# Optimization experiments

Hardware: AMD Instinct MI355X
Metric: run time of the kernel (lower is better)

## Reference

```python
import jax, jax.numpy as jnp
import numpy as np

TOP_K = 16
TAU = 1.0
LN_EPS = 1e-5
NORM_EPS = 1e-12


def setup_inputs() -> dict:
    key = jax.random.key(0)
    ks = jax.random.split(key, 8)
    B, T, V, H = 2, 1024, 32000, 1024
    inner = 2 * H
    logits = jax.random.normal(ks[0], (B, T, V), jnp.float32)
    hidden_states = jax.random.normal(ks[1], (B, T, H), jnp.float32)
    labels = jax.random.randint(ks[2], (B, T), 0, V, jnp.int32)
    future_summaries = jax.random.normal(ks[3], (B, T, H), jnp.float32)
    future_valid = jnp.ones((B, T), jnp.bool_)
    embed_weight = jax.random.normal(ks[4], (V, H), jnp.float32) * 0.02
    W1 = jax.random.normal(ks[5], (2 * H, inner), jnp.float32) * 0.02
    b1 = jnp.zeros((inner,), jnp.float32)
    W2 = jax.random.normal(ks[6], (inner, H), jnp.float32) * 0.02
    b2 = jnp.zeros((H,), jnp.float32)
    ln_g = jnp.ones((H,), jnp.float32)
    ln_b = jnp.zeros((H,), jnp.float32)
    return dict(logits=logits, hidden_states=hidden_states, labels=labels,
                future_summaries=future_summaries, future_valid=future_valid,
                embed_weight=embed_weight, W1=W1, b1=b1, W2=W2, b2=b2,
                ln_g=ln_g, ln_b=ln_b)


def _build_action_set(logits_flat, labels_flat):
    # top-k candidate ids + ground-truth id, deduped, left-packed.
    BT = logits_flat.shape[0]
    _, topk_idx = jax.lax.top_k(logits_flat, TOP_K)          # (BT, K)
    combined = jnp.concatenate([topk_idx, labels_flat[:, None]], axis=1)  # (BT, A)
    A = combined.shape[1]
    sort_order = jnp.argsort(combined, axis=1)               # stable
    sorted_idx = jnp.take_along_axis(combined, sort_order, axis=1)
    uniq_sorted = jnp.concatenate(
        [jnp.ones((BT, 1), jnp.bool_), sorted_idx[:, 1:] != sorted_idx[:, :-1]], axis=1)
    unsort = jnp.argsort(sort_order, axis=1)
    unique_mask = jnp.take_along_axis(uniq_sorted, unsort, axis=1)
    pos = jnp.cumsum(unique_mask, axis=1) - 1
    # route duplicates to a trash column A, then slice it off
    safe_pos = jnp.where(unique_mask, pos, A)
    rows = jnp.arange(BT)[:, None]
    action_indices = jnp.zeros((BT, A + 1), combined.dtype).at[rows, safe_pos].set(combined)[:, :A]
    action_mask = jnp.zeros((BT, A + 1), jnp.bool_).at[rows, safe_pos].set(True)[:, :A]
    return action_indices, action_mask


def _layernorm(x, g, b):
    mu = jnp.mean(x, axis=-1, keepdims=True)
    var = jnp.var(x, axis=-1, keepdims=True)
    return (x - mu) * jax.lax.rsqrt(var + LN_EPS) * g + b


def _normalize(x):
    n = jnp.linalg.norm(x, axis=-1, keepdims=True)
    return x / jnp.maximum(n, NORM_EPS)


def reference(logits, hidden_states, labels, future_summaries, future_valid,
              embed_weight, W1, b1, W2, b2, ln_g, ln_b):
    B, T, V = logits.shape
    H = hidden_states.shape[-1]
    logits_flat = logits.reshape(-1, V)
    hidden_flat = hidden_states.reshape(-1, H)
    labels_flat = labels.reshape(-1)
    future_flat = future_summaries.reshape(-1, H)
    valid_mask = (labels_flat != -100) & future_valid.reshape(-1)

    action_indices, action_mask = _build_action_set(
        jax.lax.stop_gradient(logits_flat), labels_flat)      # (BT, A)

    token_embeds = embed_weight[action_indices]               # (BT, A, H)
    A = token_embeds.shape[1]
    hidden_exp = jnp.broadcast_to(hidden_flat[:, None, :], token_embeds.shape)
    future_exp = jnp.broadcast_to(future_flat[:, None, :], token_embeds.shape)

    # cos_mlp head: Linear(2H, 2H) -> GELU -> Linear(2H, H) -> LayerNorm
    fused = jnp.concatenate([hidden_exp, token_embeds], axis=-1)  # (BT, A, 2H)
    h = jax.nn.gelu(jnp.einsum('baf,fi->bai', fused, W1) + b1, approximate=False)
    delta = jnp.einsum('bai,ih->bah', h, W2) + b2
    action_repr = _layernorm(delta, ln_g, ln_b)

    scores = jnp.sum(_normalize(action_repr) * _normalize(future_exp), axis=-1)  # (BT, A)
    scores = jnp.where(action_mask, scores, -1e9)
    rewards = jax.nn.softmax(scores / TAU, axis=-1) * action_mask

    act_mask_v = action_mask & valid_mask[:, None]
    log_probs = jax.nn.log_softmax(logits_flat, axis=-1)
    lp_actions = jnp.take_along_axis(log_probs, action_indices, axis=1) * act_mask_v
    loss_per_pos = -jnp.sum(jax.lax.stop_gradient(rewards) * lp_actions, axis=1)
    denom = jnp.maximum(jnp.sum(act_mask_v, axis=1), 1)
    loss_per_pos = loss_per_pos / denom * valid_mask.astype(jnp.float32)
    normalizer = jnp.maximum(jnp.sum(valid_mask.astype(jnp.float32)), 1.0)
    loss = jnp.sum(loss_per_pos) / normalizer
    return loss
```

## Files before the change

kernel.cpp:

```cpp
#include <hip/hip_runtime.h>
#include <hip/hip_bf16.h>
#include <math.h>

#define BTOT 2048
#define VV 32000
#define HH 1024
#define INNER 2048
#define NA 17
#define MTOT (BTOT * NA)
#define CAP 1088

typedef __bf16 bf16;
typedef __bf16 bf16x8 __attribute__((ext_vector_type(8)));
typedef float f32x4 __attribute__((ext_vector_type(4)));

__device__ __forceinline__ f32x4 mfma16(bf16x8 a, bf16x8 b, f32x4 c) {
    return __builtin_amdgcn_mfma_f32_16x16x32_bf16(a, b, c, 0, 0, 0);
}

__device__ __forceinline__ void gload16(const void* g, void* l) {
    __builtin_amdgcn_global_load_lds(
        (const __attribute__((address_space(1))) unsigned int*)g,
        (__attribute__((address_space(3))) unsigned int*)l, 16, 0, 0);
}

__device__ __forceinline__ bool vi_better(float va, int ia, float vb, int ib) {
    return (va > vb) || (va == vb && ia < ib);
}

__global__ __launch_bounds__(256)
void transpose_to_bf16(const float* __restrict__ src, bf16* __restrict__ dst,
                       int R, int C)
{
    __shared__ float tile[32][33];
    const int bx = blockIdx.x * 32;
    const int by = blockIdx.y * 32;
    const int tx = threadIdx.x;
    const int ty = threadIdx.y;
#pragma unroll
    for (int i = 0; i < 32; i += 8)
        tile[ty + i][tx] = src[(size_t)(by + ty + i) * C + bx + tx];
    __syncthreads();
#pragma unroll
    for (int i = 0; i < 32; i += 8)
        dst[(size_t)(bx + ty + i) * R + by + tx] = (bf16)tile[tx][ty + i];
}

__global__ __launch_bounds__(256)
void cast_hidden_kernel(const float* __restrict__ hidden, bf16* __restrict__ hb)
{
    const size_t i = ((size_t)blockIdx.x * 256 + threadIdx.x) * 8;
    float4 v0 = ((const float4*)(hidden + i))[0];
    float4 v1 = ((const float4*)(hidden + i))[1];
    bf16x8 o;
    o[0] = (bf16)v0.x; o[1] = (bf16)v0.y; o[2] = (bf16)v0.z; o[3] = (bf16)v0.w;
    o[4] = (bf16)v1.x; o[5] = (bf16)v1.y; o[6] = (bf16)v1.z; o[7] = (bf16)v1.w;
    *(bf16x8*)(hb + i) = o;
}

__global__ __launch_bounds__(256)
void topk_lse_kernel(const float* __restrict__ logits,
                     const int* __restrict__ labels,
                     const unsigned char* __restrict__ future_valid,
                     int* __restrict__ actions,
                     int* __restrict__ amask,
                     float* __restrict__ lp,
                     int* __restrict__ rvalid,
                     int* __restrict__ validcount)
{
    const int r = blockIdx.x;
    const int t = threadIdx.x;
    const float* __restrict__ lrow = logits + (size_t)r * VV;

    __shared__ float s_cv[CAP];
    __shared__ int   s_ci[CAP];
    __shared__ float candv[256];
    __shared__ int   candi[256];
    __shared__ float s_topv[16];
    __shared__ int   s_topi[16];
    __shared__ int   s_wtid;
    __shared__ int   s_cnt;
    __shared__ float s_redv[256];
    __shared__ int   s_redi[256];
    __shared__ int   s_redp[256];

    float m1 = -INFINITY, m2 = -INFINITY;
    int   i1 = 0x7fffffff, i2 = 0x7fffffff;
    const float4* __restrict__ lrow4 = (const float4*)lrow;
    for (int i = 0; i < 32; ++i) {
        int i4 = t + 256 * i;
        if (i4 < VV / 4) {
            float4 xv = lrow4[i4];
            float xs[4] = {xv.x, xv.y, xv.z, xv.w};
#pragma unroll
            for (int cc = 0; cc < 4; ++cc) {
                float x = xs[cc];
                int idx = i4 * 4 + cc;
                bool b1 = x > m1;
                bool b2 = x > m2;
                float nm2 = b1 ? m1 : (b2 ? x : m2);
                int   ni2 = b1 ? i1 : (b2 ? idx : i2);
                m1 = b1 ? x : m1;
                i1 = b1 ? idx : i1;
                m2 = nm2; i2 = ni2;
            }
        }
    }
    candv[t] = m1; candi[t] = i1;
    if (t == 0) s_cnt = 0;
    __syncthreads();

    int cur = 0;
    for (int round = 0; round < 16; ++round) {
        if (t < 64) {
            float bv = -INFINITY; int bi = 0x7fffffff; int btid = -1;
#pragma unroll
            for (int k2 = 0; k2 < 4; ++k2) {
                int tid = t + 64 * k2;
                float v = candv[tid]; int ii = candi[tid];
                if (vi_better(v, ii, bv, bi)) { bv = v; bi = ii; btid = tid; }
            }
#pragma unroll
            for (int ms = 1; ms < 64; ms <<= 1) {
                float ov = __shfl_xor(bv, ms, 64);
                int   oi = __shfl_xor(bi, ms, 64);
                int   ot = __shfl_xor(btid, ms, 64);
                if (vi_better(ov, oi, bv, bi)) { bv = ov; bi = oi; btid = ot; }
            }
            if (t == 0) { s_topv[round] = bv; s_topi[round] = bi; s_wtid = btid; }
        }
        __syncthreads();
        if (t == s_wtid) {
            ++cur;
            candv[t] = (cur < 2) ? m2 : -INFINITY;
            candi[t] = (cur < 2) ? i2 : 0x7fffffff;
        }
        __syncthreads();
    }

    const float M  = s_topv[0];
    const float Tv = s_topv[15];
    const int   Ti = s_topi[15];

    float lsum = 0.f;
    for (int i = 0; i < 32; ++i) {
        int i4 = t + 256 * i;
        if (i4 < VV / 4) {
            float4 xv = lrow4[i4];
            float xs[4] = {xv.x, xv.y, xv.z, xv.w};
#pragma unroll
            for (int cc = 0; cc < 4; ++cc) {
                float x = xs[cc];
                int idx = i4 * 4 + cc;
                lsum += __expf(x - M);
                if (!vi_better(Tv, Ti, x, idx)) {
                    int p = atomicAdd(&s_cnt, 1);
                    if (p < CAP) { s_cv[p] = x; s_ci[p] = idx; }
                }
            }
        }
    }
    s_redv[t] = lsum;
    __syncthreads();
    for (int s = 128; s > 0; s >>= 1) {
        if (t < s) s_redv[t] += s_redv[t + s];
        __syncthreads();
    }
    const float lse = M + logf(s_redv[0]);
    int C = s_cnt; if (C > CAP) C = CAP;
    __syncthreads();

    for (int round = 0; round < 16; ++round) {
        float bv = -INFINITY; int bi = 0x7fffffff; int bp = -1;
        for (int j = t; j < C; j += 256) {
            float v = s_cv[j]; int ii = s_ci[j];
            if (vi_better(v, ii, bv, bi)) { bv = v; bi = ii; bp = j; }
        }
        s_redv[t] = bv; s_redi[t] = bi; s_redp[t] = bp;
        __syncthreads();
        if (t < 64) {
#pragma unroll
            for (int k2 = 1; k2 < 4; ++k2) {
                float v = s_redv[t + 64*k2]; int ii = s_redi[t + 64*k2];
                int pp = s_redp[t + 64*k2];
                if (vi_better(v, ii, bv, bi)) { bv = v; bi = ii; bp = pp; }
            }
#pragma unroll
            for (int ms = 1; ms < 64; ms <<= 1) {
                float ov = __shfl_xor(bv, ms, 64);
                int   oi = __shfl_xor(bi, ms, 64);
                int   op = __shfl_xor(bp, ms, 64);
                if (vi_better(ov, oi, bv, bi)) { bv = ov; bi = oi; bp = op; }
            }
            if (t == 0) {
                s_topv[round] = bv; s_topi[round] = bi;
                if (bp >= 0) { s_cv[bp] = -INFINITY; s_ci[bp] = 0x7fffffff; }
            }
        }
        __syncthreads();
    }

    int lbl = labels[r];
    if (t < 16) {
        actions[r*NA + t] = s_topi[t];
        amask[r*NA + t]   = 1;
        lp[r*NA + t]      = s_topv[t] - lse;
    } else if (t == 16) {
        bool dup = false;
#pragma unroll
        for (int k = 0; k < 16; ++k) dup = dup || (s_topi[k] == lbl);
        actions[r*NA + 16] = dup ? 0 : lbl;
        amask[r*NA + 16]   = dup ? 0 : 1;
        lp[r*NA + 16]      = dup ? 0.f : (lrow[lbl] - lse);
        bool valid = (lbl != -100) && (future_valid[r] != 0);
        rvalid[r] = valid ? 1 : 0;
        if (valid) atomicAdd(validcount, 1);
    }
}

__global__ __launch_bounds__(256)
void build_embed_kernel(const float* __restrict__ embed,
                        const int* __restrict__ actions,
                        bf16* __restrict__ AE, int m0)
{
    const int t = threadIdx.x;
    const int ml = blockIdx.x * 2 + (t >> 7);
    const int gm = m0 + ml;
    const int r = gm / NA;
    const int a = gm - r * NA;
    const int tt = t & 127;
    const float* src = embed + (size_t)actions[r*NA + a] * HH + tt * 8;
    float4 v0 = ((const float4*)src)[0];
    float4 v1 = ((const float4*)src)[1];
    bf16x8 o;
    o[0] = (bf16)v0.x; o[1] = (bf16)v0.y; o[2] = (bf16)v0.z; o[3] = (bf16)v0.w;
    o[4] = (bf16)v1.x; o[5] = (bf16)v1.y; o[6] = (bf16)v1.z; o[7] = (bf16)v1.w;
    *(bf16x8*)(AE + (size_t)ml * HH + tt * 8) = o;
}

template<int MODE>
__global__ __launch_bounds__(256, 2)
void gemm128(const bf16* __restrict__ A, int lda,
             const bf16* __restrict__ Bt, int ldb, int koff, int K,
             const float* __restrict__ extra,
             bf16* __restrict__ outB, float* __restrict__ outF,
             int ldo, int nbx, int m0)
{
    const int nwg = gridDim.x;
    const int per = nwg >> 3;
    const int id  = blockIdx.x;
    const int sid = (id & 7) * per + (id >> 3);
    const int nb = sid % nbx;
    const int mb = sid / nbx;

    const int t = threadIdx.x;
    const int w = t >> 6, lane = t & 63;
    const int q = lane >> 4, c = lane & 15;
    const int wr = w >> 1, wc = w & 1;

    __shared__ __align__(16) bf16 sA[128 * 32];
    __shared__ __align__(16) bf16 sB[128 * 32];

    const int e0 = (w*2 + 0) * 512 + lane * 8;
    const int e1 = (w*2 + 1) * 512 + lane * 8;
    const bf16* gA0 = A  + (size_t)(mb*128 + (e0 >> 5)) * lda + (e0 & 31);
    const bf16* gA1 = A  + (size_t)(mb*128 + (e1 >> 5)) * lda + (e1 & 31);
    const bf16* gB0 = Bt + (size_t)(nb*128 + (e0 >> 5)) * ldb + koff + (e0 & 31);
    const bf16* gB1 = Bt + (size_t)(nb*128 + (e1 >> 5)) * ldb + koff + (e1 & 31);
    bf16* lA0 = sA + (w*2 + 0) * 512;
    bf16* lA1 = sA + (w*2 + 1) * 512;
    bf16* lB0 = sB + (w*2 + 0) * 512;
    bf16* lB1 = sB + (w*2 + 1) * 512;

    const f32x4 z4 = {0.f, 0.f, 0.f, 0.f};
    f32x4 acc[4][4];
#pragma unroll
    for (int mt = 0; mt < 4; ++mt)
#pragma unroll
        for (int nt = 0; nt < 4; ++nt) acc[mt][nt] = z4;

#pragma unroll 1
    for (int k0 = 0; k0 < K; k0 += 32) {
        gload16(gA0 + k0, lA0);
        gload16(gA1 + k0, lA1);
        gload16(gB0 + k0, lB0);
        gload16(gB1 + k0, lB1);
        __syncthreads();

        bf16x8 af[4], bfr[4];
#pragma unroll
        for (int mt = 0; mt < 4; ++mt)
            af[mt] = *(const bf16x8*)&sA[(wr*64 + mt*16 + c) * 32 + q*8];
#pragma unroll
        for (int nt = 0; nt < 4; ++nt)
            bfr[nt] = *(const bf16x8*)&sB[(wc*64 + nt*16 + c) * 32 + q*8];
#pragma unroll
        for (int mt = 0; mt < 4; ++mt)
#pragma unroll
            for (int nt = 0; nt < 4; ++nt)
                acc[mt][nt] = mfma16(af[mt], bfr[nt], acc[mt][nt]);
        __syncthreads();
    }

    const int mrow = mb*128 + wr*64;
    const int ncol = nb*128 + wc*64;
#pragma unroll
    for (int nt = 0; nt < 4; ++nt) {
        const int n = ncol + nt*16 + c;
        float bb = 0.f;
        if constexpr (MODE == 2) bb = extra[n];
#pragma unroll
        for (int mt = 0; mt < 4; ++mt) {
#pragma unroll
            for (int reg = 0; reg < 4; ++reg) {
                const int m = mrow + mt*16 + q*4 + reg;
                float x = acc[mt][nt][reg];
                if constexpr (MODE == 0) {
                    outF[(size_t)m * ldo + n] = x;
                } else if constexpr (MODE == 1) {
                    const int gr = (m0 + m) / NA;
                    x += extra[(size_t)gr * INNER + n];
                    const float g = 0.5f * x * (1.f + erff(x * 0.70710678118654752f));
                    outB[(size_t)m * ldo + n] = (bf16)g;
                } else {
                    outF[(size_t)m * ldo + n] = x + bb;
                }
            }
        }
    }
}

__global__ __launch_bounds__(256)
void ln_cos_kernel(const float* __restrict__ D,
                   const float* __restrict__ b2,
                   const float* __restrict__ ln_g,
                   const float* __restrict__ ln_b,
                   const float* __restrict__ future,
                   int m0,
                   float* __restrict__ scores)
{
    const int ml = blockIdx.x;
    const int m = m0 + ml;
    const int r = m / NA;
    const int t = threadIdx.x;
    const int w = t >> 6, lane = t & 63;
    __shared__ float s1[4], s2[4], s3[4], s4[4], s5[4];

    float4 d  = ((const float4*)(D + (size_t)ml * HH))[t];
    float4 bb = ((const float4*)b2)[t];
    d.x += bb.x; d.y += bb.y; d.z += bb.z; d.w += bb.w;

    float p1 = d.x + d.y + d.z + d.w;
    float p2 = d.x*d.x + d.y*d.y + d.z*d.z + d.w*d.w;
#pragma unroll
    for (int m2 = 1; m2 < 64; m2 <<= 1) {
        p1 += __shfl_xor(p1, m2, 64);
        p2 += __shfl_xor(p2, m2, 64);
    }
    if (lane == 0) { s1[w] = p1; s2[w] = p2; }
    __syncthreads();
    const float S1 = s1[0] + s1[1] + s1[2] + s1[3];
    const float S2 = s2[0] + s2[1] + s2[2] + s2[3];
    const float mu = S1 * (1.f / (float)HH);
    const float rstd = rsqrtf(S2 * (1.f / (float)HH) - mu*mu + 1e-5f);

    float4 g = ((const float4*)ln_g)[t];
    float4 b = ((const float4*)ln_b)[t];
    float4 f = ((const float4*)(future + (size_t)r * HH))[t];
    float4 ar;
    ar.x = (d.x - mu) * rstd * g.x + b.x;
    ar.y = (d.y - mu) * rstd * g.y + b.y;
    ar.z = (d.z - mu) * rstd * g.z + b.z;
    ar.w = (d.w - mu) * rstd * g.w + b.w;
    float paa = ar.x*ar.x + ar.y*ar.y + ar.z*ar.z + ar.w*ar.w;
    float paf = ar.x*f.x  + ar.y*f.y  + ar.z*f.z  + ar.w*f.w;
    float pff = f.x*f.x   + f.y*f.y   + f.z*f.z   + f.w*f.w;
#pragma unroll
    for (int m2 = 1; m2 < 64; m2 <<= 1) {
        paa += __shfl_xor(paa, m2, 64);
        paf += __shfl_xor(paf, m2, 64);
        pff += __shfl_xor(pff, m2, 64);
    }
    if (lane == 0) { s3[w] = paa; s4[w] = paf; s5[w] = pff; }
    __syncthreads();
    if (t == 0) {
        const float Saa = s3[0] + s3[1] + s3[2] + s3[3];
        const float Saf = s4[0] + s4[1] + s4[2] + s4[3];
        const float Sff = s5[0] + s5[1] + s5[2] + s5[3];
        const float anorm = fmaxf(sqrtf(Saa), 1e-12f);
        const float fnorm = fmaxf(sqrtf(Sff), 1e-12f);
        scores[m] = Saf / (anorm * fnorm);
    }
}

__global__ __launch_bounds__(256)
void loss_kernel(const float* __restrict__ scores,
                 const int* __restrict__ amask,
                 const float* __restrict__ lp,
                 const int* __restrict__ rvalid,
                 const int* __restrict__ validcount,
                 float* __restrict__ out)
{
    const int r = blockIdx.x * blockDim.x + threadIdx.x;
    if (r >= BTOT) return;
    float sc[NA];
    float mx = -INFINITY;
#pragma unroll
    for (int a = 0; a < NA; ++a) {
        sc[a] = amask[r*NA + a] ? scores[r*NA + a] : -1e9f;
        mx = fmaxf(mx, sc[a]);
    }
    float ex[NA]; float ses = 0.f;
#pragma unroll
    for (int a = 0; a < NA; ++a) { ex[a] = __expf(sc[a] - mx); ses += ex[a]; }
    const int validr = rvalid[r];
    float acc = 0.f; int denom = 0;
#pragma unroll
    for (int a = 0; a < NA; ++a) {
        const int mk = amask[r*NA + a];
        const int mv = (mk && validr) ? 1 : 0;
        const float rw = (ex[a] / ses) * (float)mk;
        acc += rw * lp[r*NA + a] * (float)mv;
        denom += mv;
    }
    const float lossr = -acc / (float)(denom > 0 ? denom : 1) * (float)validr;
    atomicAdd(out, lossr / fmaxf((float)(*validcount), 1.f));
}

extern "C" void kernel_launch(void* const* d_in, const int* in_sizes, int n_in,
                              void* d_out, int out_size, void* d_ws, size_t ws_size,
                              hipStream_t stream)
{
    const float* logits        = (const float*)d_in[0];
    const float* hidden        = (const float*)d_in[1];
    const int*   labels        = (const int*)d_in[2];
    const float* future        = (const float*)d_in[3];
    const unsigned char* fvld  = (const unsigned char*)d_in[4];
    const float* embed         = (const float*)d_in[5];
    const float* W1f           = (const float*)d_in[6];
    const float* b1            = (const float*)d_in[7];
    const float* W2f           = (const float*)d_in[8];
    const float* b2            = (const float*)d_in[9];
    const float* ln_g          = (const float*)d_in[10];
    const float* ln_b          = (const float*)d_in[11];
    float* out = (float*)d_out;

    char* ws = (char*)d_ws;
    size_t off = 0;
    bf16*  W1T   = (bf16*)(ws + off);  off += (size_t)INNER * INNER * 2;
    bf16*  W2T   = (bf16*)(ws + off);  off += (size_t)HH * INNER * 2;
    bf16*  hidB  = (bf16*)(ws + off);  off += (size_t)BTOT * HH * 2;
    float* Hpre  = (float*)(ws + off); off += (size_t)BTOT * INNER * 4;
    int*   validcount = (int*)(ws + off);   off += 256;
    int*   actions    = (int*)(ws + off);   off += (size_t)MTOT * 4;
    int*   amask      = (int*)(ws + off);   off += (size_t)MTOT * 4;
    float* lp         = (float*)(ws + off); off += (size_t)MTOT * 4;
    int*   rvalid     = (int*)(ws + off);   off += (size_t)BTOT * 4;
    float* scores     = (float*)(ws + off); off += (size_t)MTOT * 4;
    off = (off + 255) & ~(size_t)255;

    size_t rem = (ws_size > off) ? (ws_size - off) : 0;
    long long cap_blocks = (long long)(rem / ((size_t)10240 * 128));
    int slab_blocks = (cap_blocks > (MTOT/128)) ? (MTOT/128) : (int)cap_blocks;
    if (slab_blocks < 1) slab_blocks = 1;
    const int slab_rows_max = slab_blocks * 128;

    bf16*  AEbuf = (bf16*)(ws + off);
    bf16*  Ybuf  = (bf16*)(ws + off + (size_t)slab_rows_max * 2048);
    float* Dbuf  = (float*)(ws + off + (size_t)slab_rows_max * (2048 + 4096));

    (void)hipMemsetAsync(d_out, 0, sizeof(float), stream);
    (void)hipMemsetAsync(validcount, 0, 16, stream);

    transpose_to_bf16<<<dim3(INNER/32, INNER/32), dim3(32, 8), 0, stream>>>(W1f, W1T, INNER, INNER);
    transpose_to_bf16<<<dim3(HH/32,    INNER/32), dim3(32, 8), 0, stream>>>(W2f, W2T, INNER, HH);
    cast_hidden_kernel<<<(BTOT*HH)/2048, 256, 0, stream>>>(hidden, hidB);

    gemm128<2><<<(INNER/128) * (BTOT/128), 256, 0, stream>>>(
        hidB, HH, W1T, INNER, 0, HH, b1, nullptr, Hpre, INNER, INNER/128, 0);

    topk_lse_kernel<<<BTOT, 256, 0, stream>>>(logits, labels, fvld,
                                              actions, amask, lp, rvalid, validcount);

    for (int m0 = 0; m0 < MTOT; m0 += slab_rows_max) {
        const int rows = (MTOT - m0 < slab_rows_max) ? (MTOT - m0) : slab_rows_max;
        const int nbm = rows / 128;
        build_embed_kernel<<<rows/2, 256, 0, stream>>>(embed, actions, AEbuf, m0);
        gemm128<1><<<(INNER/128) * nbm, 256, 0, stream>>>(
            AEbuf, HH, W1T, INNER, HH, HH, Hpre, Ybuf, nullptr, INNER, INNER/128, m0);
        gemm128<0><<<(HH/128) * nbm, 256, 0, stream>>>(
            Ybuf, INNER, W2T, INNER, 0, INNER, nullptr, nullptr, Dbuf, HH, HH/128, 0);
        ln_cos_kernel<<<rows, 256, 0, stream>>>(Dbuf, b2, ln_g, ln_b, future, m0, scores);
    }

    loss_kernel<<<(BTOT + 255) / 256, 256, 0, stream>>>(scores, amask, lp,
                                                        rvalid, validcount, out);
}
```

Baseline: 1.111 ms.

## Triple-buffer GEMM LDS tiles with async prefetch and XOR-swizzled layout

Replaces the single-buffered load/sync/compute loop in gemm128 with a 3-stage LDS ring buffer. Tiles are prefetched two iterations ahead using global_load_lds, and progress is tracked with explicit vmcnt waits and raw s_barrier calls. It also swizzles the column placement of each 16-byte chunk per row to reduce LDS bank conflicts on fragment reads. The aim is to hide global memory latency behind MFMA work, at the cost of tripling LDS use (lower occupancy) and relying on hand-written waitcnt correctness.

```diff
diff --git a/kernel.cpp b/kernel.cpp
--- a/kernel.cpp
+++ b/kernel.cpp
@@ -258,19 +258,24 @@
     const int q = lane >> 4, c = lane & 15;
     const int wr = w >> 1, wc = w & 1;
 
-    __shared__ __align__(16) bf16 sA[128 * 32];
-    __shared__ __align__(16) bf16 sB[128 * 32];
-
-    const int e0 = (w*2 + 0) * 512 + lane * 8;
-    const int e1 = (w*2 + 1) * 512 + lane * 8;
-    const bf16* gA0 = A  + (size_t)(mb*128 + (e0 >> 5)) * lda + (e0 & 31);
-    const bf16* gA1 = A  + (size_t)(mb*128 + (e1 >> 5)) * lda + (e1 & 31);
-    const bf16* gB0 = Bt + (size_t)(nb*128 + (e0 >> 5)) * ldb + koff + (e0 & 31);
-    const bf16* gB1 = Bt + (size_t)(nb*128 + (e1 >> 5)) * ldb + koff + (e1 & 31);
-    bf16* lA0 = sA + (w*2 + 0) * 512;
-    bf16* lA1 = sA + (w*2 + 1) * 512;
-    bf16* lB0 = sB + (w*2 + 0) * 512;
-    bf16* lB1 = sB + (w*2 + 1) * 512;
+    __shared__ __align__(16) bf16 sAB[3][2][128 * 32];
+
+    const int sl = (lane & ~3) | ((lane & 3) ^ ((lane >> 3) & 3));
+    const int j0 = w * 2, j1 = w * 2 + 1;
+    const int srow0 = j0 * 16 + (sl >> 2);
+    const int srow1 = j1 * 16 + (sl >> 2);
+    const int scol  = (sl & 3) * 8;
+    const bf16* gA0 = A  + (size_t)(mb*128 + srow0) * lda + scol;
+    const bf16* gA1 = A  + (size_t)(mb*128 + srow1) * lda + scol;
+    const bf16* gB0 = Bt + (size_t)(nb*128 + srow0) * ldb + koff + scol;
+    const bf16* gB1 = Bt + (size_t)(nb*128 + srow1) * ldb + koff + scol;
+
+    auto STAGE = [&](int b, int kk) {
+        gload16(gA0 + kk, &sAB[b][0][j0 * 512]);
+        gload16(gA1 + kk, &sAB[b][0][j1 * 512]);
+        gload16(gB0 + kk, &sAB[b][1][j0 * 512]);
+        gload16(gB1 + kk, &sAB[b][1][j1 * 512]);
+    };
 
     const f32x4 z4 = {0.f, 0.f, 0.f, 0.f};
     f32x4 acc[4][4];
@@ -279,27 +284,41 @@
 #pragma unroll
         for (int nt = 0; nt < 4; ++nt) acc[mt][nt] = z4;
 
+    const int nk = K >> 5;
+    STAGE(0, 0);
+    if (nk > 1) STAGE(1, 32);
+
+    const int qe = (q ^ ((c >> 1) & 3)) * 8;
+
 #pragma unroll 1
-    for (int k0 = 0; k0 < K; k0 += 32) {
-        gload16(gA0 + k0, lA0);
-        gload16(gA1 + k0, lA1);
-        gload16(gB0 + k0, lB0);
-        gload16(gB1 + k0, lB1);
-        __syncthreads();
-
+    for (int i = 0; i < nk; ++i) {
+        const int b = i % 3;
+        if (i + 2 < nk) STAGE((i + 2) % 3, (i + 2) * 32);
+
+        const int rem = nk - 1 - i;
+        if (rem >= 2)      asm volatile("s_waitcnt vmcnt(8)" ::: "memory");
+        else if (rem == 1) asm volatile("s_waitcnt vmcnt(4)" ::: "memory");
+        else               asm volatile("s_waitcnt vmcnt(0)" ::: "memory");
+        __builtin_amdgcn_s_barrier();
+        asm volatile("" ::: "memory");
+
+        const bf16* baseA = &sAB[b][0][0];
+        const bf16* baseB = &sAB[b][1][0];
         bf16x8 af[4], bfr[4];
 #pragma unroll
         for (int mt = 0; mt < 4; ++mt)
-            af[mt] = *(const bf16x8*)&sA[(wr*64 + mt*16 + c) * 32 + q*8];
+            af[mt] = *(const bf16x8*)&baseA[(wr*4 + mt) * 512 + c * 32 + qe];
 #pragma unroll
         for (int nt = 0; nt < 4; ++nt)
-            bfr[nt] = *(const bf16x8*)&sB[(wc*64 + nt*16 + c) * 32 + q*8];
+            bfr[nt] = *(const bf16x8*)&baseB[(wc*4 + nt) * 512 + c * 32 + qe];
 #pragma unroll
         for (int mt = 0; mt < 4; ++mt)
 #pragma unroll
             for (int nt = 0; nt < 4; ++nt)
                 acc[mt][nt] = mfma16(af[mt], bfr[nt], acc[mt][nt]);
-        __syncthreads();
+
+        asm volatile("" ::: "memory");
+        __builtin_amdgcn_s_barrier();
     }
 
     const int mrow = mb*128 + wr*64;
```

New measurement: 1.091 ms. About the same (-1.8%).
